# Optimization experiments

Hardware: AMD Instinct MI355X
Metric: run time of the kernel (lower is better)

The kernel has to match this reference:

```python
import jax, jax.numpy as jnp
import numpy as np

N_NODES = 40000
N_EDGES = 640000
IN_CH = 128
HID_CH = 128
OUT_CH = 121


def setup_inputs() -> dict:
    key = jax.random.key(0)
    ks = jax.random.split(key, 6)
    x = jax.random.normal(ks[0], (N_NODES, IN_CH), dtype=jnp.float32)
    edge_index = jax.random.randint(ks[1], (2, N_EDGES), 0, N_NODES, dtype=jnp.int64)

    def xavier(k, shape):
        fan_out, fan_in = shape
        lim = np.sqrt(6.0 / (fan_in + fan_out)).astype(np.float32)
        return jax.random.uniform(k, shape, jnp.float32, -lim, lim)

    W1l = xavier(ks[2], (HID_CH, IN_CH))
    W1r = xavier(ks[3], (HID_CH, IN_CH))
    W2l = xavier(ks[4], (OUT_CH, HID_CH))
    W2r = xavier(ks[5], (OUT_CH, HID_CH))
    b1l = jnp.zeros((HID_CH,), jnp.float32)
    b1r = jnp.zeros((HID_CH,), jnp.float32)
    b2l = jnp.zeros((OUT_CH,), jnp.float32)
    b2r = jnp.zeros((OUT_CH,), jnp.float32)
    return {"x": x, "edge_index": edge_index,
            "W1l": W1l, "b1l": b1l, "W1r": W1r, "b1r": b1r,
            "W2l": W2l, "b2l": b2l, "W2r": W2r, "b2r": b2r}


def _sage_conv(h, src, dst, Wl, bl, Wr, br):
    # mean aggregation of source-node features onto destinations
    msg = h[src]                                             # [E, C]
    agg = jax.ops.segment_sum(msg, dst, num_segments=N_NODES)
    cnt = jax.ops.segment_sum(jnp.ones((src.shape[0],), h.dtype), dst,
                              num_segments=N_NODES)
    agg = agg / jnp.maximum(cnt, 1.0)[:, None]
    # out = lin_l(agg) + lin_r(h)
    return agg @ Wl.T + bl + h @ Wr.T + br


def reference(x, edge_index, W1l, b1l, W1r, b1r, W2l, b2l, W2r, b2r):
    src, dst = edge_index[0], edge_index[1]
    h = jax.nn.relu(_sage_conv(x, src, dst, W1l, b1l, W1r, b1r))
    # dropout is identity in inference mode
    return _sage_conv(h, src, dst, W2l, b2l, W2r, b2r)
```

## Files before the change

### kernel.cpp

```cpp
#include <hip/hip_runtime.h>
#include <hip/hip_fp8.h>


#define NCH 128
#define CAPX 16
#define EPT 8

typedef __bf16 bf16x8 __attribute__((ext_vector_type(8)));
typedef float f32x4 __attribute__((ext_vector_type(4)));
typedef unsigned char uchar8 __attribute__((ext_vector_type(8)));

static __device__ __forceinline__ unsigned short f2b(float f) {
  return __builtin_bit_cast(unsigned short, static_cast<__bf16>(f));
}
static __device__ __forceinline__ unsigned char f2q(float f) {
  __hip_fp8_e4m3 q(f);
  return (unsigned char)q.__x;
}
static __device__ __forceinline__ float q2f(unsigned char b) {
  __hip_fp8_e4m3 q;
  q.__x = (__hip_fp8_storage_t)b;
  return (float)q;
}

__global__ __launch_bounds__(256) void k_main(
    const int* __restrict__ src, const int* __restrict__ dst, int E,
    int* __restrict__ cntx, unsigned short* __restrict__ slotu,
    int* __restrict__ ovf_n, int2* __restrict__ ovf,
    const float* __restrict__ x, unsigned short* __restrict__ xb,
    unsigned char* __restrict__ x8, int n4,
    const float* __restrict__ W1l, const float* __restrict__ W1r,
    const float* __restrict__ b1l, const float* __restrict__ b1r,
    const float* __restrict__ W2l, const float* __restrict__ W2r,
    const float* __restrict__ b2l, const float* __restrict__ b2r,
    unsigned short* __restrict__ pack1, unsigned short* __restrict__ pack2,
    float* __restrict__ bsum1, float* __restrict__ bsum2, int NOUT,
    int nbBkt, int nbCvt) {
  int blk = blockIdx.x;
  if (blk < nbBkt) {
    unsigned int xcc;
    asm volatile("s_getreg_b32 %0, hwreg(HW_REG_XCC_ID)" : "=s"(xcc));
    xcc &= 7u;
    const int base = blk * (256 * EPT) + (int)threadIdx.x;
    int d[EPT], s[EPT], pos[EPT];
#pragma unroll
    for (int j = 0; j < EPT; ++j) {
      const int e = base + j * 256;
      const bool ok = e < E;
      d[j] = ok ? dst[e] : -1;
      s[j] = ok ? src[e] : 0;
    }
#pragma unroll
    for (int j = 0; j < EPT; ++j) {
      pos[j] = (d[j] >= 0)
          ? __hip_atomic_fetch_add(&cntx[(long)d[j] * 8 + xcc], 1,
                                   __ATOMIC_RELAXED, __HIP_MEMORY_SCOPE_WORKGROUP)
          : 0;
    }
#pragma unroll
    for (int j = 0; j < EPT; ++j) {
      if (d[j] >= 0) {
        if (pos[j] < CAPX)
          slotu[(long)d[j] * 128 + xcc * CAPX + pos[j]] = (unsigned short)s[j];
        else {
          int o = atomicAdd(ovf_n, 1);
          ovf[o] = make_int2(d[j], s[j]);
        }
      }
    }
    return;
  }
  blk -= nbBkt;
  if (blk < nbCvt) {
    int i = blk * 256 + threadIdx.x;
    if (i < n4) {
      float4 v = ((const float4*)x)[i];
      ushort4 r;
      r.x = f2b(v.x); r.y = f2b(v.y); r.z = f2b(v.z); r.w = f2b(v.w);
      ((ushort4*)xb)[i] = r;
      uchar4 q;
      q.x = f2q(v.x); q.y = f2q(v.y); q.z = f2q(v.z); q.w = f2q(v.w);
      ((uchar4*)x8)[i] = q;
    }
    return;
  }
  blk -= nbCvt;
  const int layer = blk >> 4;
  const float* Wl = layer ? W2l : W1l;
  const float* Wr = layer ? W2r : W1r;
  const float* bl = layer ? b2l : b1l;
  const float* br = layer ? b2r : b1r;
  unsigned short* pack = layer ? pack2 : pack1;
  float* bsum = layer ? bsum2 : bsum1;
  const int NO = layer ? NOUT : NCH;
  int tid = (blk & 15) * 256 + threadIdx.x;
  int c = tid >> 9;
  int t = (tid >> 6) & 7;
  int l = tid & 63;
  int n = t * 16 + (l & 15);
  int kb = c * 32 + ((l >> 4) << 3);
  unsigned short o[8];
#pragma unroll
  for (int j = 0; j < 8; ++j) {
    int k = kb + j;
    float v = 0.f;
    if (n < NO) v = (k < 128) ? Wl[n * 128 + k] : Wr[n * 128 + (k - 128)];
    o[j] = f2b(v);
  }
  ushort4 lo, hi;
  lo.x = o[0]; lo.y = o[1]; lo.z = o[2]; lo.w = o[3];
  hi.x = o[4]; hi.y = o[5]; hi.z = o[6]; hi.w = o[7];
  *(ushort4*)(pack + (long)tid * 8) = lo;
  *(ushort4*)(pack + (long)tid * 8 + 4) = hi;
  if (tid < 128) bsum[tid] = (tid < NO) ? (bl[tid] + br[tid]) : 0.f;
}

__global__ __launch_bounds__(256) void k_agg(
    const unsigned char* __restrict__ feat8, const int* __restrict__ cntx,
    const unsigned short* __restrict__ slotu, const int* __restrict__ ovf_n,
    const int2* __restrict__ ovf, unsigned short* __restrict__ agg, int N) {
  __shared__ unsigned short list[16][128];
  __shared__ float lut[256];
  __shared__ int degs[16], ms[16];
  const int lg = threadIdx.x >> 4;
  const int ln = threadIdx.x & 15;
  const int g = blockIdx.x * 16 + lg;

  lut[threadIdx.x] = q2f((unsigned char)threadIdx.x);

  if (g < N) {
    const int4 cA = *(const int4*)(cntx + (long)g * 8);
    const int4 cB = *(const int4*)(cntx + (long)g * 8 + 4);
    const int c[8] = {cA.x, cA.y, cA.z, cA.w, cB.x, cB.y, cB.z, cB.w};
    int deg = 0, p = 0, myoff = 0, mycc = 0;
#pragma unroll
    for (int xx = 0; xx < 8; ++xx) {
      const int cc = (c[xx] < CAPX) ? c[xx] : CAPX;
      if (ln == xx) { myoff = p; mycc = cc; }
      p += cc;
      deg += c[xx];
    }
    if (ln == 0) { degs[lg] = deg; ms[lg] = p; }
    if (ln < 8 && mycc > 0) {
      const unsigned short* sp = slotu + (long)g * 128 + ln * CAPX;
      for (int i = 0; i < mycc; ++i) list[lg][myoff + i] = sp[i];
    }
  } else if (ln == 0) {
    degs[lg] = 0; ms[lg] = 0;
  }
  __syncthreads();

  if (g >= N) return;
  const int m = ms[lg];
  const int col = ln * 8;
  const unsigned char* fcol = feat8 + col;

  float acc[8];
#pragma unroll
  for (int k = 0; k < 8; ++k) acc[k] = 0.f;

  const unsigned short* __restrict__ il = list[lg];
  int j = 0;
  for (; j + 7 < m; j += 8) {
    const int i0 = il[j + 0], i1 = il[j + 1], i2 = il[j + 2], i3 = il[j + 3];
    const int i4 = il[j + 4], i5 = il[j + 5], i6 = il[j + 6], i7 = il[j + 7];
    const uchar8 v0 = *(const uchar8*)(fcol + (long)i0 * NCH);
    const uchar8 v1 = *(const uchar8*)(fcol + (long)i1 * NCH);
    const uchar8 v2 = *(const uchar8*)(fcol + (long)i2 * NCH);
    const uchar8 v3 = *(const uchar8*)(fcol + (long)i3 * NCH);
    const uchar8 v4 = *(const uchar8*)(fcol + (long)i4 * NCH);
    const uchar8 v5 = *(const uchar8*)(fcol + (long)i5 * NCH);
    const uchar8 v6 = *(const uchar8*)(fcol + (long)i6 * NCH);
    const uchar8 v7 = *(const uchar8*)(fcol + (long)i7 * NCH);
#pragma unroll
    for (int k = 0; k < 8; ++k) {
      acc[k] += lut[v0[k]]; acc[k] += lut[v1[k]];
      acc[k] += lut[v2[k]]; acc[k] += lut[v3[k]];
      acc[k] += lut[v4[k]]; acc[k] += lut[v5[k]];
      acc[k] += lut[v6[k]]; acc[k] += lut[v7[k]];
    }
  }
  if (j + 3 < m) {
    const int i0 = il[j + 0], i1 = il[j + 1], i2 = il[j + 2], i3 = il[j + 3];
    const uchar8 v0 = *(const uchar8*)(fcol + (long)i0 * NCH);
    const uchar8 v1 = *(const uchar8*)(fcol + (long)i1 * NCH);
    const uchar8 v2 = *(const uchar8*)(fcol + (long)i2 * NCH);
    const uchar8 v3 = *(const uchar8*)(fcol + (long)i3 * NCH);
#pragma unroll
    for (int k = 0; k < 8; ++k) {
      acc[k] += lut[v0[k]]; acc[k] += lut[v1[k]];
      acc[k] += lut[v2[k]]; acc[k] += lut[v3[k]];
    }
    j += 4;
  }
  for (; j < m; ++j) {
    const uchar8 v = *(const uchar8*)(fcol + (long)il[j] * NCH);
#pragma unroll
    for (int k = 0; k < 8; ++k) acc[k] += lut[v[k]];
  }

  const int on = *ovf_n;
  for (int o = 0; o < on; ++o) {
    const int2 p = ovf[o];
    if (p.x == g) {
      const uchar8 v = *(const uchar8*)(fcol + (long)p.y * NCH);
#pragma unroll
      for (int k = 0; k < 8; ++k) acc[k] += lut[v[k]];
    }
  }

  const int deg = degs[lg];
  const int dd = (deg < 1) ? 1 : deg;
  const float inv = 1.f / (float)dd;
  ushort4 rlo, rhi;
  rlo.x = f2b(acc[0] * inv); rlo.y = f2b(acc[1] * inv);
  rlo.z = f2b(acc[2] * inv); rlo.w = f2b(acc[3] * inv);
  rhi.x = f2b(acc[4] * inv); rhi.y = f2b(acc[5] * inv);
  rhi.z = f2b(acc[6] * inv); rhi.w = f2b(acc[7] * inv);
  *(ushort4*)(agg + (long)g * NCH + col) = rlo;
  *(ushort4*)(agg + (long)g * NCH + col + 4) = rhi;
}

__global__ __launch_bounds__(256) void k_gemm(
    const unsigned short* __restrict__ Ag,
    const unsigned short* __restrict__ Sf,
    const unsigned short* __restrict__ pack,
    const float* __restrict__ bsum,
    unsigned short* __restrict__ outb,
    unsigned char* __restrict__ out8,
    float* __restrict__ outf,
    int M, int NO, int do_relu) {
  const int wave = threadIdx.x >> 6;
  const int lane = threadIdx.x & 63;
  const int R = blockIdx.x * 128 + wave * 32;
  const int mrow = lane & 15;
  const int koct = (lane >> 4) * 8;

  int r0 = R + mrow;       if (r0 > M - 1) r0 = M - 1;
  int r1 = R + 16 + mrow;  if (r1 > M - 1) r1 = M - 1;

  f32x4 acc[2][8];
#pragma unroll
  for (int mt = 0; mt < 2; ++mt)
#pragma unroll
    for (int t = 0; t < 8; ++t) acc[mt][t] = (f32x4){0.f, 0.f, 0.f, 0.f};

#pragma unroll
  for (int c = 0; c < 8; ++c) {
    const unsigned short* __restrict__ Abase = (c < 4) ? Ag : Sf;
    const int k0 = (c & 3) * 32;
    const bf16x8 a0 = *(const bf16x8*)(Abase + (long)r0 * NCH + k0 + koct);
    const bf16x8 a1 = *(const bf16x8*)(Abase + (long)r1 * NCH + k0 + koct);
    const unsigned short* bp = pack + ((long)(c * 8) * 64 + lane) * 8;
#pragma unroll
    for (int t = 0; t < 8; ++t) {
      const bf16x8 bfrag = *(const bf16x8*)(bp + (long)t * 512);
      acc[0][t] = __builtin_amdgcn_mfma_f32_16x16x32_bf16(a0, bfrag, acc[0][t], 0, 0, 0);
      acc[1][t] = __builtin_amdgcn_mfma_f32_16x16x32_bf16(a1, bfrag, acc[1][t], 0, 0, 0);
    }
  }

  const int nloc = lane & 15;
  const int rquad = (lane >> 4) * 4;
#pragma unroll
  for (int mt = 0; mt < 2; ++mt) {
#pragma unroll
    for (int t = 0; t < 8; ++t) {
      const int n = t * 16 + nloc;
      const float bias = bsum[n];
#pragma unroll
      for (int r = 0; r < 4; ++r) {
        const int m = R + mt * 16 + rquad + r;
        if (m < M && n < NO) {
          float v = acc[mt][t][r] + bias;
          if (do_relu) v = fmaxf(v, 0.f);
          if (outb) {
            outb[(long)m * NCH + n] = f2b(v);
            out8[(long)m * NCH + n] = f2q(v);
          } else {
            outf[(long)m * NO + n] = v;
          }
        }
      }
    }
  }
}


extern "C" void kernel_launch(void* const* d_in, const int* in_sizes, int n_in,
                              void* d_out, int out_size, void* d_ws, size_t ws_size,
                              hipStream_t stream) {
  const float* x = (const float*)d_in[0];
  const int* ei = (const int*)d_in[1];
  const float* W1l = (const float*)d_in[2];
  const float* b1l = (const float*)d_in[3];
  const float* W1r = (const float*)d_in[4];
  const float* b1r = (const float*)d_in[5];
  const float* W2l = (const float*)d_in[6];
  const float* b2l = (const float*)d_in[7];
  const float* W2r = (const float*)d_in[8];
  const float* b2r = (const float*)d_in[9];
  float* out = (float*)d_out;

  const int N = in_sizes[0] / NCH;
  const int E = in_sizes[1] / 2;
  const int NOUT = out_size / N;

  const int* src = ei;
  const int* dst = ei + E;

  char* w = (char*)d_ws;
  auto alloc = [&](size_t bytes) {
    char* p = w;
    w += (bytes + 255) & ~(size_t)255;
    return p;
  };
  unsigned short* xb = (unsigned short*)alloc((size_t)N * NCH * 2);
  unsigned short* hb = (unsigned short*)alloc((size_t)N * NCH * 2);
  unsigned short* aggb = (unsigned short*)alloc((size_t)N * NCH * 2);
  unsigned char* x8 = (unsigned char*)alloc((size_t)N * NCH);
  unsigned char* h8 = (unsigned char*)alloc((size_t)N * NCH);
  unsigned short* pack1 = (unsigned short*)alloc(8 * 8 * 64 * 8 * 2);
  unsigned short* pack2 = (unsigned short*)alloc(8 * 8 * 64 * 8 * 2);
  float* bsum1 = (float*)alloc(128 * 4);
  float* bsum2 = (float*)alloc(128 * 4);
  int* cntx = (int*)alloc(((size_t)N * 8 + 4) * 4);
  int* ovf_n = cntx + (size_t)N * 8;
  unsigned short* slotu = (unsigned short*)alloc((size_t)N * 128 * 2);
  int2* ovf = (int2*)alloc((size_t)E * 8);

  const int n4 = N * NCH / 4;
  const int nbBkt = (E + 256 * EPT - 1) / (256 * EPT);
  const int nbCvt = (n4 + 255) / 256;

  hipMemsetAsync(cntx, 0, ((size_t)N * 8 + 4) * 4, stream);

  k_main<<<nbBkt + nbCvt + 32, 256, 0, stream>>>(
      src, dst, E, cntx, slotu, ovf_n, ovf,
      x, xb, x8, n4,
      W1l, W1r, b1l, b1r, W2l, W2r, b2l, b2r,
      pack1, pack2, bsum1, bsum2, NOUT, nbBkt, nbCvt);

  const int gaggr = (N + 15) / 16;
  const int gblk = (N + 127) / 128;

  k_agg<<<gaggr, 256, 0, stream>>>(x8, cntx, slotu, ovf_n, ovf, aggb, N);
  k_gemm<<<gblk, 256, 0, stream>>>(aggb, xb, pack1, bsum1, hb, h8,
                                   (float*)nullptr, N, NCH, 1);
  k_agg<<<gaggr, 256, 0, stream>>>(h8, cntx, slotu, ovf_n, ovf, aggb, N);
  k_gemm<<<gblk, 256, 0, stream>>>(aggb, hb, pack2, bsum2,
                                   (unsigned short*)nullptr, (unsigned char*)nullptr,
                                   out, N, NOUT, 0);
}
```

Baseline: 204.8 us.

## Use XCC-major count and slot layouts, halve per-XCC capacity, add nontemporal I/O

The per-node counters and slot lists move from node-major with 8 interleaved XCC sub-buckets to XCC-major arrays, so each XCC's atomics and slot writes land in a separate contiguous region instead of sharing cache lines. The per-XCC slot capacity drops from 16 to 8, which halves the slot buffer and the shared list, at the cost of more edges going to the overflow path on high-degree nodes. The edge loads and the x conversion loads and stores become nontemporal, and the aggregation kernel now stages the counts through shared memory with an extra barrier.

Result: slower. 229.2 us (+11.9%).

```diff
diff --git a/kernel.cpp b/kernel.cpp
--- a/kernel.cpp
+++ b/kernel.cpp
@@ -3,12 +3,15 @@
 
 
 #define NCH 128
-#define CAPX 16
+#define CAPX 8
 #define EPT 8
 
 typedef __bf16 bf16x8 __attribute__((ext_vector_type(8)));
 typedef float f32x4 __attribute__((ext_vector_type(4)));
 typedef unsigned char uchar8 __attribute__((ext_vector_type(8)));
+typedef float f32x4v __attribute__((ext_vector_type(4)));
+typedef unsigned short u16x4v __attribute__((ext_vector_type(4)));
+typedef unsigned char u8x4v __attribute__((ext_vector_type(4)));
 
 static __device__ __forceinline__ unsigned short f2b(float f) {
   return __builtin_bit_cast(unsigned short, static_cast<__bf16>(f));
@@ -35,25 +38,27 @@
     const float* __restrict__ b2l, const float* __restrict__ b2r,
     unsigned short* __restrict__ pack1, unsigned short* __restrict__ pack2,
     float* __restrict__ bsum1, float* __restrict__ bsum2, int NOUT,
-    int nbBkt, int nbCvt) {
+    int nbBkt, int nbCvt, int Nn) {
   int blk = blockIdx.x;
   if (blk < nbBkt) {
     unsigned int xcc;
     asm volatile("s_getreg_b32 %0, hwreg(HW_REG_XCC_ID)" : "=s"(xcc));
     xcc &= 7u;
+    const long cbase = (long)xcc * Nn;
+    const long lbase = (long)xcc * Nn * CAPX;
     const int base = blk * (256 * EPT) + (int)threadIdx.x;
     int d[EPT], s[EPT], pos[EPT];
 #pragma unroll
     for (int j = 0; j < EPT; ++j) {
       const int e = base + j * 256;
       const bool ok = e < E;
-      d[j] = ok ? dst[e] : -1;
-      s[j] = ok ? src[e] : 0;
+      d[j] = ok ? __builtin_nontemporal_load(dst + e) : -1;
+      s[j] = ok ? __builtin_nontemporal_load(src + e) : 0;
     }
 #pragma unroll
     for (int j = 0; j < EPT; ++j) {
       pos[j] = (d[j] >= 0)
-          ? __hip_atomic_fetch_add(&cntx[(long)d[j] * 8 + xcc], 1,
+          ? __hip_atomic_fetch_add(&cntx[cbase + d[j]], 1,
                                    __ATOMIC_RELAXED, __HIP_MEMORY_SCOPE_WORKGROUP)
           : 0;
     }
@@ -61,7 +66,7 @@
     for (int j = 0; j < EPT; ++j) {
       if (d[j] >= 0) {
         if (pos[j] < CAPX)
-          slotu[(long)d[j] * 128 + xcc * CAPX + pos[j]] = (unsigned short)s[j];
+          slotu[lbase + (long)d[j] * CAPX + pos[j]] = (unsigned short)s[j];
         else {
           int o = atomicAdd(ovf_n, 1);
           ovf[o] = make_int2(d[j], s[j]);
@@ -74,13 +79,13 @@
   if (blk < nbCvt) {
     int i = blk * 256 + threadIdx.x;
     if (i < n4) {
-      float4 v = ((const float4*)x)[i];
-      ushort4 r;
+      const f32x4v v = __builtin_nontemporal_load((const f32x4v*)x + i);
+      u16x4v r;
       r.x = f2b(v.x); r.y = f2b(v.y); r.z = f2b(v.z); r.w = f2b(v.w);
-      ((ushort4*)xb)[i] = r;
-      uchar4 q;
+      __builtin_nontemporal_store(r, (u16x4v*)xb + i);
+      u8x4v q;
       q.x = f2q(v.x); q.y = f2q(v.y); q.z = f2q(v.z); q.w = f2q(v.w);
-      ((uchar4*)x8)[i] = q;
+      __builtin_nontemporal_store(q, (u8x4v*)x8 + i);
     }
     return;
   }
@@ -119,30 +124,37 @@
     const unsigned char* __restrict__ feat8, const int* __restrict__ cntx,
     const unsigned short* __restrict__ slotu, const int* __restrict__ ovf_n,
     const int2* __restrict__ ovf, unsigned short* __restrict__ agg, int N) {
-  __shared__ unsigned short list[16][128];
+  __shared__ unsigned short list[16][64];
   __shared__ float lut[256];
   __shared__ int degs[16], ms[16];
+  __shared__ int cnts[16][8];
   const int lg = threadIdx.x >> 4;
   const int ln = threadIdx.x & 15;
   const int g = blockIdx.x * 16 + lg;
 
   lut[threadIdx.x] = q2f((unsigned char)threadIdx.x);
 
+  if (threadIdx.x < 128) {
+    const int xx = threadIdx.x >> 4;
+    const int lgg = threadIdx.x & 15;
+    const int gg = blockIdx.x * 16 + lgg;
+    cnts[lgg][xx] = (gg < N) ? cntx[(long)xx * N + gg] : 0;
+  }
+  __syncthreads();
+
   if (g < N) {
-    const int4 cA = *(const int4*)(cntx + (long)g * 8);
-    const int4 cB = *(const int4*)(cntx + (long)g * 8 + 4);
-    const int c[8] = {cA.x, cA.y, cA.z, cA.w, cB.x, cB.y, cB.z, cB.w};
     int deg = 0, p = 0, myoff = 0, mycc = 0;
 #pragma unroll
     for (int xx = 0; xx < 8; ++xx) {
-      const int cc = (c[xx] < CAPX) ? c[xx] : CAPX;
+      const int cv = cnts[lg][xx];
+      const int cc = (cv < CAPX) ? cv : CAPX;
       if (ln == xx) { myoff = p; mycc = cc; }
       p += cc;
-      deg += c[xx];
+      deg += cv;
     }
     if (ln == 0) { degs[lg] = deg; ms[lg] = p; }
     if (ln < 8 && mycc > 0) {
-      const unsigned short* sp = slotu + (long)g * 128 + ln * CAPX;
+      const unsigned short* sp = slotu + ((long)ln * N + g) * CAPX;
       for (int i = 0; i < mycc; ++i) list[lg][myoff + i] = sp[i];
     }
   } else if (ln == 0) {
@@ -326,7 +338,7 @@
   float* bsum2 = (float*)alloc(128 * 4);
   int* cntx = (int*)alloc(((size_t)N * 8 + 4) * 4);
   int* ovf_n = cntx + (size_t)N * 8;
-  unsigned short* slotu = (unsigned short*)alloc((size_t)N * 128 * 2);
+  unsigned short* slotu = (unsigned short*)alloc((size_t)N * 8 * CAPX * 2);
   int2* ovf = (int2*)alloc((size_t)E * 8);
 
   const int n4 = N * NCH / 4;
@@ -339,7 +351,7 @@
       src, dst, E, cntx, slotu, ovf_n, ovf,
       x, xb, x8, n4,
       W1l, W1r, b1l, b1r, W2l, W2r, b2l, b2r,
-      pack1, pack2, bsum1, bsum2, NOUT, nbBkt, nbCvt);
+      pack1, pack2, bsum1, bsum2, NOUT, nbBkt, nbCvt, N);
 
   const int gaggr = (N + 15) / 16;
   const int gblk = (N + 127) / 128;
```
